# Kernel tuning notes

Hardware: AMD Instinct MI355X
Metric: run time of the kernel (lower is better)

Reference implementation:

```python
import jax, jax.numpy as jnp
import numpy as np

B, S, D, H = 4, 2048, 512, 16
HD = D // H          # head_dim = 32
ROPE_DIM = HD        # rope_pct = 1.0
NEG = -1e30


def apply_rope(x):
    # x: [B, H, S, HD]; rotate first ROPE_DIM dims, half-split (NeoX) convention
    half = ROPE_DIM // 2
    pos = jnp.arange(S, dtype=jnp.float32)
    inv_freq = 1.0 / (10000.0 ** (jnp.arange(0, ROPE_DIM, 2, dtype=jnp.float32) / ROPE_DIM))
    ang = pos[:, None] * inv_freq[None, :]          # [S, half]
    cos, sin = jnp.cos(ang), jnp.sin(ang)           # broadcast over B,H
    x1 = x[..., :half]
    x2 = x[..., half:ROPE_DIM]
    r1 = x1 * cos - x2 * sin
    r2 = x2 * cos + x1 * sin
    rest = x[..., ROPE_DIM:]
    return jnp.concatenate([r1, r2, rest], axis=-1)


def setup_inputs() -> dict:
    key = jax.random.key(0)
    ks = jax.random.split(key, 7)
    x = jax.random.normal(ks[0], (B, S, D), dtype=jnp.float32)
    # causal mask: True = block (j > i)
    attn_mask = jnp.triu(jnp.ones((S, S), dtype=bool), k=1)
    # padding mask: True = PAD; random lengths in [S//2, S]
    lengths = jax.random.randint(ks[1], (B,), S // 2, S + 1)
    key_padding_mask = jnp.arange(S)[None, :] >= lengths[:, None]
    scale = D ** -0.5
    Wq = jax.random.normal(ks[2], (D, D), dtype=jnp.float32) * scale
    Wk = jax.random.normal(ks[3], (D, D), dtype=jnp.float32) * scale
    Wv = jax.random.normal(ks[4], (D, D), dtype=jnp.float32) * scale
    Wo = jax.random.normal(ks[5], (D, D), dtype=jnp.float32) * scale
    return {"x": x, "attn_mask": attn_mask, "key_padding_mask": key_padding_mask,
            "Wq": Wq, "Wk": Wk, "Wv": Wv, "Wo": Wo}


def reference(x, attn_mask, key_padding_mask, Wq, Wk, Wv, Wo):
    scale = HD ** -0.5
    # nn.Linear: y = x @ W.T
    q = (x @ Wq.T).reshape(B, S, H, HD).transpose(0, 2, 1, 3)  # [B,H,S,HD]
    k = (x @ Wk.T).reshape(B, S, H, HD).transpose(0, 2, 1, 3)
    v = (x @ Wv.T).reshape(B, S, H, HD).transpose(0, 2, 1, 3)
    q = apply_rope(q)
    k = apply_rope(k)
    scores = jnp.einsum('bhid,bhjd->bhij', q, k) * scale       # [B,H,S,S]
    scores = jnp.where(key_padding_mask[:, None, None, :], NEG, scores)
    scores = jnp.where(attn_mask[None, None, :, :], NEG, scores)
    probs = jax.nn.softmax(scores.astype(jnp.float32), axis=-1)
    probs = jnp.nan_to_num(probs, nan=0.0)
    ctx = jnp.einsum('bhij,bhjd->bhid', probs, v)              # [B,H,S,HD]
    ctx = ctx.transpose(0, 2, 1, 3).reshape(B, S, D)
    ctx = jnp.where(key_padding_mask[:, :, None], 0.0, ctx)
    return ctx @ Wo.T
```

## Files before the change

### kernel.cpp

```cpp
#include <hip/hip_runtime.h>
#include <hip/hip_bf16.h>

#define B_ 4
#define S_ 2048
#define D_ 512
#define H_ 16
#define HD_ 32

typedef __bf16 bf16;
typedef __bf16 bf16x4 __attribute__((ext_vector_type(4)));
typedef __bf16 bf16x8 __attribute__((ext_vector_type(8)));
typedef float f32x4 __attribute__((ext_vector_type(4)));

__device__ __forceinline__ f32x4 mfma16(bf16x8 a, bf16x8 b, f32x4 c) {
  return __builtin_amdgcn_mfma_f32_16x16x32_bf16(a, b, c, 0, 0, 0);
}

__device__ __forceinline__ void gload16(const bf16* g, bf16* l) {
  __builtin_amdgcn_global_load_lds(
      (const __attribute__((address_space(1))) void*)g,
      (__attribute__((address_space(3))) void*)l, 16, 0, 0);
}

__device__ __forceinline__ bf16x8 cvt8(const float* __restrict__ p) {
  const f32x4* v = (const f32x4*)p;
  f32x4 a = v[0], b = v[1];
  bf16x8 r;
  r[0] = (bf16)a[0]; r[1] = (bf16)a[1]; r[2] = (bf16)a[2]; r[3] = (bf16)a[3];
  r[4] = (bf16)b[0]; r[5] = (bf16)b[1]; r[6] = (bf16)b[2]; r[7] = (bf16)b[3];
  return r;
}

__global__ __launch_bounds__(256) void prep_kernel(
    const float* __restrict__ x, const float* __restrict__ wq,
    const float* __restrict__ wk, const float* __restrict__ wv,
    const float* __restrict__ wo, const unsigned char* __restrict__ am,
    const unsigned char* __restrict__ kpm, bf16* __restrict__ xb,
    bf16* __restrict__ dq, bf16* __restrict__ dk, bf16* __restrict__ dv,
    bf16* __restrict__ dwo, int* __restrict__ lengths_out,
    float* __restrict__ costab, float* __restrict__ sintab) {
  int bid = blockIdx.x;
  if (bid < 2048) {
    size_t i = (size_t)bid * 256 + threadIdx.x;
    *(bf16x8*)(xb + i * 8) = cvt8(x + i * 8);
  } else if (bid < 2560) {
    int wb = bid - 2048;
    int mat = wb >> 7;
    size_t i = (size_t)(wb & 127) * 256 + threadIdx.x;
    const float* s = (mat == 0) ? wq : (mat == 1) ? wk : (mat == 2) ? wv : wo;
    bf16* d = (mat == 0) ? dq : (mat == 1) ? dk : (mat == 2) ? dv : dwo;
    *(bf16x8*)(d + i * 8) = cvt8(s + i * 8);
  } else if (bid == 2560) {
    int b = threadIdx.x >> 6, lane = threadIdx.x & 63;
    int esize;
    if (am[1] == 1) esize = 1;
    else if (am[2] == 0x80 && am[3] == 0x3F) esize = 2;
    else if (am[3] == 0x3C) esize = 2;
    else if (am[4] == 1) esize = 4;
    else if (am[6] == 0x80 && am[7] == 0x3F) esize = 4;
    else if (am[8] == 1) esize = 8;
    else esize = 1;
    int cnt = 0;
    for (int i = lane; i < S_; i += 64) {
      size_t off = ((size_t)b * S_ + i) * (size_t)esize;
      unsigned char nz = 0;
      for (int e = 0; e < esize; ++e) nz |= kpm[off + e];
      cnt += (nz == 0) ? 1 : 0;
    }
    for (int off = 1; off < 64; off <<= 1) cnt += __shfl_xor(cnt, off);
    if (lane == 0) lengths_out[b] = cnt;
  } else {
    int ti = (bid - 2561) * 256 + threadIdx.x;
    int s = ti >> 4, cc = ti & 15;
    float invf = powf(10000.0f, -(float)cc * (1.0f / 16.0f));
    float ang = (float)s * invf;
    costab[ti] = cosf(ang);
    sintab[ti] = sinf(ang);
  }
}

#define LDT 136
__global__ __launch_bounds__(256) void qkv_rope_kernel(
    const bf16* __restrict__ x, const bf16* __restrict__ Wq,
    const bf16* __restrict__ Wk, const bf16* __restrict__ Wv,
    const float* __restrict__ costab, const float* __restrict__ sintab,
    bf16* __restrict__ q_ws, bf16* __restrict__ k_ws, bf16* __restrict__ vt_ws) {
  __shared__ __align__(16) bf16 smem[17408];
#define AS(b) (smem + (b) * 4096)
#define BS(b) (smem + 8192 + (b) * 4096)
#define CT smem

  int bid = blockIdx.x;
  int brow = bid / 12, bc = bid % 12;
  int mat = bc >> 2;
  const bf16* W = (mat == 0) ? Wq : (mat == 1) ? Wk : Wv;
  int row0 = brow * 128;
  int col0 = (bc & 3) * 128;

  int tid = threadIdx.x;
  int w = tid >> 6, l = tid & 63;
  int wr = w >> 1, wc = w & 1;
  int g = l >> 4, c = l & 15;
  int lrow = l >> 2;
  int lcol = (l & 3) * 8;

  f32x4 acc[4][4];
  f32x4 zero = {0.f, 0.f, 0.f, 0.f};
#pragma unroll
  for (int m = 0; m < 4; ++m)
#pragma unroll
    for (int n = 0; n < 4; ++n) acc[m][n] = zero;

#pragma unroll
  for (int j = 0; j < 2; ++j) {
    int chunk = w * 2 + j;
    int grow = chunk * 16 + lrow;
    gload16(x + (size_t)(row0 + grow) * 512 + lcol, AS(0) + chunk * 512);
    gload16(W + (size_t)(col0 + grow) * 512 + lcol, BS(0) + chunk * 512);
  }
  __syncthreads();
  int cur = 0;

#pragma unroll 1
  for (int k0 = 0; k0 < 512; k0 += 32) {
    bool more = (k0 < 480);
    if (more) {
#pragma unroll
      for (int j = 0; j < 2; ++j) {
        int chunk = w * 2 + j;
        int grow = chunk * 16 + lrow;
        gload16(x + (size_t)(row0 + grow) * 512 + k0 + 32 + lcol,
                AS(cur ^ 1) + chunk * 512);
        gload16(W + (size_t)(col0 + grow) * 512 + k0 + 32 + lcol,
                BS(cur ^ 1) + chunk * 512);
      }
    }
    bf16x8 af[4], bfr[4];
#pragma unroll
    for (int m = 0; m < 4; ++m)
      af[m] = *(const bf16x8*)(AS(cur) + (wr * 64 + m * 16 + c) * 32 + g * 8);
#pragma unroll
    for (int n = 0; n < 4; ++n)
      bfr[n] = *(const bf16x8*)(BS(cur) + (wc * 64 + n * 16 + c) * 32 + g * 8);
#pragma unroll
    for (int m = 0; m < 4; ++m)
#pragma unroll
      for (int n = 0; n < 4; ++n) acc[m][n] = mfma16(af[m], bfr[n], acc[m][n]);
    if (more) {
      __syncthreads();
      cur ^= 1;
    }
  }

  if (mat < 2) {
    bf16* dst = (mat == 0) ? q_ws : k_ws;
    const float esc =
        (mat == 0) ? (0.17677669529663687f * 1.4426950408889634f) : 1.0f;
#pragma unroll
    for (int m = 0; m < 4; ++m) {
      int rbase = row0 + wr * 64 + m * 16 + g * 4;
#pragma unroll
      for (int r = 0; r < 4; ++r) {
        int grow = rbase + r;
        int bb = grow >> 11, s = grow & (S_ - 1);
        float cs = costab[s * 16 + c];
        float sn = sintab[s * 16 + c];
#pragma unroll
        for (int np = 0; np < 2; ++np) {
          int n = np * 2;
          int obase = col0 + wc * 64 + n * 16;
          int h = obase >> 5;
          float a0 = acc[m][n][r], a1 = acc[m][n + 1][r];
          size_t base = (((size_t)bb * H_ + h) * S_ + s) * HD_;
          dst[base + c] = (bf16)((a0 * cs - a1 * sn) * esc);
          dst[base + c + 16] = (bf16)((a1 * cs + a0 * sn) * esc);
        }
      }
    }
  } else {
    __syncthreads();
#pragma unroll
    for (int m = 0; m < 4; ++m) {
#pragma unroll
      for (int n = 0; n < 4; ++n) {
        int o = wc * 64 + n * 16 + c;
        int sb = wr * 64 + m * 16 + g * 4;
        bf16x4 q4;
        q4[0] = (bf16)acc[m][n][0]; q4[1] = (bf16)acc[m][n][1];
        q4[2] = (bf16)acc[m][n][2]; q4[3] = (bf16)acc[m][n][3];
        *(bf16x4*)(&CT[o * LDT + sb]) = q4;
      }
    }
    __syncthreads();
    int o_l = tid >> 1, sh = (tid & 1) * 64;
    int o = col0 + o_l;
    int h = o >> 5, hd = o & 31;
    int bb2 = row0 >> 11, sr = row0 & (S_ - 1);
    size_t dst = (((size_t)bb2 * H_ + h) * HD_ + hd) * S_ + sr + sh;
#pragma unroll
    for (int j = 0; j < 8; ++j)
      *(bf16x8*)(vt_ws + dst + j * 8) =
          *(const bf16x8*)(&CT[o_l * LDT + sh + j * 8]);
  }
#undef AS
#undef BS
#undef CT
}

__global__ __launch_bounds__(256) void attn_kernel(
    const bf16* __restrict__ q_ws, const bf16* __restrict__ k_ws,
    const bf16* __restrict__ vt_ws, const int* __restrict__ lengths,
    bf16* __restrict__ ctx_ws) {
  __shared__ __align__(16) bf16 Ks[2][2048];
  __shared__ __align__(16) bf16 Vts[2][2048];
  __shared__ __align__(16) bf16 Ps[4][1024];

  int p = blockIdx.x;
  int bh = blockIdx.y;
  int bb = bh >> 4, h = bh & 15;
  int tid = threadIdx.x, w = tid >> 6, l = tid & 63, g = l >> 4, c = l & 15;
  const size_t bh_base = ((size_t)bb * H_ + h) * (size_t)S_ * HD_;
  int len = lengths[bb];
  int rowrel = w * 16 + c;

  int srowK = w * 16 + (l & 15), skgK = l >> 4;
  int srowV = w * 8 + (l & 7), ssgV = l >> 3;
  int slotK8 = (skgK * 16 + (srowK & 15) + ((srowK >> 4) << 6)) * 8;
  int slotV8 =
      ((ssgV & 3) * 16 + (srowV & 15) + (((ssgV >> 2) + ((srowV >> 4) << 1)) << 6)) * 8;

  bf16 one = (bf16)1.0f;
  bf16x8 onesf;
#pragma unroll
  for (int i = 0; i < 8; ++i) onesf[i] = one;

#pragma unroll 1
  for (int phase = 0; phase < 2; ++phase) {
    int qt = phase ? (31 - p) : p;
    int q0 = qt * 64 + w * 16;

    bf16x8 qf = *(const bf16x8*)(q_ws + bh_base + (size_t)(q0 + c) * HD_ + g * 8);

    f32x4 zero = {0.f, 0.f, 0.f, 0.f};
    f32x4 ctxa[2];
    ctxa[0] = zero; ctxa[1] = zero;
    f32x4 lsum = zero;

    const bf16* kptr = k_ws + bh_base + (size_t)srowK * HD_ + skgK * 8;
    const bf16* vptr = vt_ws + bh_base + (size_t)srowV * S_ + ssgV * 8;

    bf16x8 regK = *(const bf16x8*)kptr;
    bf16x8 regV = *(const bf16x8*)vptr;
    kptr += 64 * HD_;
    vptr += 64;
    __syncthreads();
    *(bf16x8*)(&Ks[0][slotK8]) = regK;
    *(bf16x8*)(&Vts[0][slotV8]) = regV;
    __syncthreads();
    int cur = 0;

#pragma unroll 1
    for (int kt = 0; kt <= qt; ++kt) {
      bool hasNext = (kt < qt);
      if (hasNext) {
        regK = *(const bf16x8*)kptr;
        regV = *(const bf16x8*)vptr;
        kptr += 64 * HD_;
        vptr += 64;
      }
      const bf16* KsC = Ks[cur];
      const bf16* VtsC = Vts[cur];

      f32x4 sacc[4];
#pragma unroll
      for (int n = 0; n < 4; ++n) {
        bf16x8 kf = *(const bf16x8*)(&KsC[(l + (n << 6)) * 8]);
        sacc[n] = mfma16(kf, qf, zero);
      }

      float sv[4][4];
      if (kt != qt) {
#pragma unroll
        for (int n = 0; n < 4; ++n)
#pragma unroll
          for (int r = 0; r < 4; ++r)
            sv[n][r] = __builtin_amdgcn_exp2f(sacc[n][r]);
      } else {
#pragma unroll
        for (int n = 0; n < 4; ++n) {
          int jr = n * 16 + g * 4;
#pragma unroll
          for (int r = 0; r < 4; ++r) {
            float e = __builtin_amdgcn_exp2f(sacc[n][r]);
            sv[n][r] = (jr + r > rowrel) ? 0.f : e;
          }
        }
      }

#pragma unroll
      for (int n = 0; n < 4; ++n) {
        bf16x4 pk;
        pk[0] = (bf16)sv[n][0]; pk[1] = (bf16)sv[n][1];
        pk[2] = (bf16)sv[n][2]; pk[3] = (bf16)sv[n][3];
        int chunk = 2 * n + (g >> 1);
        int off = ((chunk >> 2) << 9) + ((chunk & 3) * 16 + c) * 8 + ((g & 1) << 2);
        *(bf16x4*)(&Ps[w][off]) = pk;
      }

      bf16x8 pf0 = *(const bf16x8*)(&Ps[w][l * 8]);
      bf16x8 pf1 = *(const bf16x8*)(&Ps[w][512 + l * 8]);

      lsum = mfma16(pf0, onesf, lsum);
      lsum = mfma16(pf1, onesf, lsum);

#pragma unroll
      for (int n2 = 0; n2 < 2; ++n2) {
        bf16x8 v0 = *(const bf16x8*)(&VtsC[(l + ((2 * n2) << 6)) * 8]);
        bf16x8 v1 = *(const bf16x8*)(&VtsC[(l + ((1 + 2 * n2) << 6)) * 8]);
        ctxa[n2] = mfma16(pf0, v0, ctxa[n2]);
        ctxa[n2] = mfma16(pf1, v1, ctxa[n2]);
      }

      if (hasNext) {
        *(bf16x8*)(&Ks[cur ^ 1][slotK8]) = regK;
        *(bf16x8*)(&Vts[cur ^ 1][slotV8]) = regV;
        __syncthreads();
        cur ^= 1;
      }
    }

#pragma unroll
    for (int n = 0; n < 2; ++n)
#pragma unroll
      for (int r = 0; r < 4; ++r) {
        int qr = q0 + g * 4 + r;
        float val = ctxa[n][r] / lsum[r];
        if (qr >= len) val = 0.f;
        ctx_ws[(((size_t)bb * S_ + qr) * H_ + h) * HD_ + n * 16 + c] = (bf16)val;
      }
  }
}

__global__ __launch_bounds__(256) void out_proj_kernel(
    const bf16* __restrict__ ctx, const bf16* __restrict__ Wo,
    float* __restrict__ out) {
  __shared__ __align__(16) bf16 As[2][4096];
  __shared__ __align__(16) bf16 Bs[2][4096];

  int bid = blockIdx.x;
  int brow = bid >> 2, bc = bid & 3;
  int row0 = brow * 128, col0 = bc * 128;
  int tid = threadIdx.x;
  int w = tid >> 6, l = tid & 63;
  int wr = w >> 1, wc = w & 1;
  int g = l >> 4, c = l & 15;
  int lrow = l >> 2;
  int lcol = (l & 3) * 8;

  f32x4 acc[4][4];
  f32x4 zero = {0.f, 0.f, 0.f, 0.f};
#pragma unroll
  for (int m = 0; m < 4; ++m)
#pragma unroll
    for (int n = 0; n < 4; ++n) acc[m][n] = zero;

#pragma unroll
  for (int j = 0; j < 2; ++j) {
    int chunk = w * 2 + j;
    int grow = chunk * 16 + lrow;
    gload16(ctx + (size_t)(row0 + grow) * 512 + lcol, As[0] + chunk * 512);
    gload16(Wo + (size_t)(col0 + grow) * 512 + lcol, Bs[0] + chunk * 512);
  }
  __syncthreads();
  int cur = 0;

#pragma unroll 1
  for (int k0 = 0; k0 < 512; k0 += 32) {
    bool more = (k0 < 480);
    if (more) {
#pragma unroll
      for (int j = 0; j < 2; ++j) {
        int chunk = w * 2 + j;
        int grow = chunk * 16 + lrow;
        gload16(ctx + (size_t)(row0 + grow) * 512 + k0 + 32 + lcol,
                As[cur ^ 1] + chunk * 512);
        gload16(Wo + (size_t)(col0 + grow) * 512 + k0 + 32 + lcol,
                Bs[cur ^ 1] + chunk * 512);
      }
    }
    bf16x8 af[4], bfr[4];
#pragma unroll
    for (int m = 0; m < 4; ++m)
      af[m] = *(const bf16x8*)(As[cur] + (wr * 64 + m * 16 + c) * 32 + g * 8);
#pragma unroll
    for (int n = 0; n < 4; ++n)
      bfr[n] = *(const bf16x8*)(Bs[cur] + (wc * 64 + n * 16 + c) * 32 + g * 8);
#pragma unroll
    for (int m = 0; m < 4; ++m)
#pragma unroll
      for (int n = 0; n < 4; ++n) acc[m][n] = mfma16(af[m], bfr[n], acc[m][n]);
    if (more) {
      __syncthreads();
      cur ^= 1;
    }
  }

#pragma unroll
  for (int m = 0; m < 4; ++m) {
    int rbase = row0 + wr * 64 + m * 16 + g * 4;
#pragma unroll
    for (int n = 0; n < 4; ++n) {
      int o = col0 + wc * 64 + n * 16 + c;
#pragma unroll
      for (int r = 0; r < 4; ++r)
        out[(size_t)(rbase + r) * 512 + o] = acc[m][n][r];
    }
  }
}

extern "C" void kernel_launch(void* const* d_in, const int* in_sizes, int n_in,
                              void* d_out, int out_size, void* d_ws,
                              size_t ws_size, hipStream_t stream) {
  const float* x = (const float*)d_in[0];
  const unsigned char* am = (const unsigned char*)d_in[1];
  const unsigned char* kpm = (const unsigned char*)d_in[2];
  const float* Wq = (const float*)d_in[3];
  const float* Wk = (const float*)d_in[4];
  const float* Wv = (const float*)d_in[5];
  const float* Wo = (const float*)d_in[6];
  float* out = (float*)d_out;

  char* ws = (char*)d_ws;
  int* lengths = (int*)ws;
  const size_t QKV_ELEMS = (size_t)B_ * H_ * S_ * HD_;
  const size_t W_ELEMS = (size_t)D_ * D_;
  bf16* xb = (bf16*)(ws + 256);
  bf16* q_ws = xb + QKV_ELEMS;
  bf16* k_ws = q_ws + QKV_ELEMS;
  bf16* vt_ws = k_ws + QKV_ELEMS;
  bf16* wqb = vt_ws + QKV_ELEMS;
  bf16* wkb = wqb + W_ELEMS;
  bf16* wvb = wkb + W_ELEMS;
  bf16* wob = wvb + W_ELEMS;
  float* costab = (float*)(wob + W_ELEMS);
  float* sintab = costab + (size_t)S_ * 16;
  bf16* ctx_ws = xb;

  hipLaunchKernelGGL(prep_kernel, dim3(2689), dim3(256), 0, stream, x, Wq, Wk,
                     Wv, Wo, am, kpm, xb, wqb, wkb, wvb, wob, lengths, costab,
                     sintab);
  hipLaunchKernelGGL(qkv_rope_kernel, dim3(768), dim3(256), 0, stream, xb, wqb,
                     wkb, wvb, costab, sintab, q_ws, k_ws, vt_ws);
  hipLaunchKernelGGL(attn_kernel, dim3(16, 64), dim3(256), 0, stream, q_ws, k_ws,
                     vt_ws, lengths, ctx_ws);
  hipLaunchKernelGGL(out_proj_kernel, dim3(256), dim3(256), 0, stream, ctx_ws,
                     wob, out);
}
```

Before: 122.0 us.

## Stage two KV tiles per barrier in attention; halve out-proj row tile

```diff
diff --git a/kernel.cpp b/kernel.cpp
--- a/kernel.cpp
+++ b/kernel.cpp
@@ -211,8 +211,8 @@
     const bf16* __restrict__ q_ws, const bf16* __restrict__ k_ws,
     const bf16* __restrict__ vt_ws, const int* __restrict__ lengths,
     bf16* __restrict__ ctx_ws) {
-  __shared__ __align__(16) bf16 Ks[2][2048];
-  __shared__ __align__(16) bf16 Vts[2][2048];
+  __shared__ __align__(16) bf16 Ks[2][4096];
+  __shared__ __align__(16) bf16 Vts[2][4096];
   __shared__ __align__(16) bf16 Ps[4][1024];
 
   int p = blockIdx.x;
@@ -238,6 +238,7 @@
   for (int phase = 0; phase < 2; ++phase) {
     int qt = phase ? (31 - p) : p;
     int q0 = qt * 64 + w * 16;
+    int T = qt + 1;
 
     bf16x8 qf = *(const bf16x8*)(q_ws + bh_base + (size_t)(q0 + c) * HD_ + g * 8);
 
@@ -246,31 +247,27 @@
     ctxa[0] = zero; ctxa[1] = zero;
     f32x4 lsum = zero;
 
-    const bf16* kptr = k_ws + bh_base + (size_t)srowK * HD_ + skgK * 8;
-    const bf16* vptr = vt_ws + bh_base + (size_t)srowV * S_ + ssgV * 8;
-
-    bf16x8 regK = *(const bf16x8*)kptr;
-    bf16x8 regV = *(const bf16x8*)vptr;
-    kptr += 64 * HD_;
-    vptr += 64;
+    const bf16* kbase = k_ws + bh_base + (size_t)srowK * HD_ + skgK * 8;
+    const bf16* vbase = vt_ws + bh_base + (size_t)srowV * S_ + ssgV * 8;
+
+    bf16x8 rK0 = *(const bf16x8*)kbase;
+    bf16x8 rV0 = *(const bf16x8*)vbase;
+    bf16x8 rK1 = rK0, rV1 = rV0;
+    if (T > 1) {
+      rK1 = *(const bf16x8*)(kbase + 64 * HD_);
+      rV1 = *(const bf16x8*)(vbase + 64);
+    }
     __syncthreads();
-    *(bf16x8*)(&Ks[0][slotK8]) = regK;
-    *(bf16x8*)(&Vts[0][slotV8]) = regV;
+    *(bf16x8*)(&Ks[0][slotK8]) = rK0;
+    *(bf16x8*)(&Vts[0][slotV8]) = rV0;
+    *(bf16x8*)(&Ks[0][2048 + slotK8]) = rK1;
+    *(bf16x8*)(&Vts[0][2048 + slotV8]) = rV1;
     __syncthreads();
     int cur = 0;
 
-#pragma unroll 1
-    for (int kt = 0; kt <= qt; ++kt) {
-      bool hasNext = (kt < qt);
-      if (hasNext) {
-        regK = *(const bf16x8*)kptr;
-        regV = *(const bf16x8*)vptr;
-        kptr += 64 * HD_;
-        vptr += 64;
-      }
-      const bf16* KsC = Ks[cur];
-      const bf16* VtsC = Vts[cur];
-
+    auto body = [&](int t, int off) {
+      const bf16* KsC = &Ks[cur][off];
+      const bf16* VtsC = &Vts[cur][off];
       f32x4 sacc[4];
 #pragma unroll
       for (int n = 0; n < 4; ++n) {
@@ -279,7 +276,7 @@
       }
 
       float sv[4][4];
-      if (kt != qt) {
+      if (t != qt) {
 #pragma unroll
         for (int n = 0; n < 4; ++n)
 #pragma unroll
@@ -303,8 +300,8 @@
         pk[0] = (bf16)sv[n][0]; pk[1] = (bf16)sv[n][1];
         pk[2] = (bf16)sv[n][2]; pk[3] = (bf16)sv[n][3];
         int chunk = 2 * n + (g >> 1);
-        int off = ((chunk >> 2) << 9) + ((chunk & 3) * 16 + c) * 8 + ((g & 1) << 2);
-        *(bf16x4*)(&Ps[w][off]) = pk;
+        int poff = ((chunk >> 2) << 9) + ((chunk & 3) * 16 + c) * 8 + ((g & 1) << 2);
+        *(bf16x4*)(&Ps[w][poff]) = pk;
       }
 
       bf16x8 pf0 = *(const bf16x8*)(&Ps[w][l * 8]);
@@ -320,13 +317,29 @@
         ctxa[n2] = mfma16(pf0, v0, ctxa[n2]);
         ctxa[n2] = mfma16(pf1, v1, ctxa[n2]);
       }
-
-      if (hasNext) {
-        *(bf16x8*)(&Ks[cur ^ 1][slotK8]) = regK;
-        *(bf16x8*)(&Vts[cur ^ 1][slotV8]) = regV;
-        __syncthreads();
-        cur ^= 1;
-      }
+    };
+
+#pragma unroll 1
+    for (int r = 0;; ++r) {
+      int t0 = 2 * r, t1 = 2 * r + 1;
+      bool more = (t0 + 2 < T);
+      if (more) {
+        const bf16* kp = kbase + (size_t)(t0 + 2) * 64 * HD_;
+        const bf16* vp = vbase + (t0 + 2) * 64;
+        rK0 = *(const bf16x8*)kp;
+        rV0 = *(const bf16x8*)vp;
+        rK1 = *(const bf16x8*)(kp + 64 * HD_);
+        rV1 = *(const bf16x8*)(vp + 64);
+      }
+      body(t0, 0);
+      if (t1 < T) body(t1, 2048);
+      if (!more) break;
+      *(bf16x8*)(&Ks[cur ^ 1][slotK8]) = rK0;
+      *(bf16x8*)(&Vts[cur ^ 1][slotV8]) = rV0;
+      *(bf16x8*)(&Ks[cur ^ 1][2048 + slotK8]) = rK1;
+      *(bf16x8*)(&Vts[cur ^ 1][2048 + slotV8]) = rV1;
+      __syncthreads();
+      cur ^= 1;
     }
 
 #pragma unroll
@@ -344,12 +357,12 @@
 __global__ __launch_bounds__(256) void out_proj_kernel(
     const bf16* __restrict__ ctx, const bf16* __restrict__ Wo,
     float* __restrict__ out) {
-  __shared__ __align__(16) bf16 As[2][4096];
+  __shared__ __align__(16) bf16 As[2][2048];
   __shared__ __align__(16) bf16 Bs[2][4096];
 
   int bid = blockIdx.x;
   int brow = bid >> 2, bc = bid & 3;
-  int row0 = brow * 128, col0 = bc * 128;
+  int row0 = brow * 64, col0 = bc * 128;
   int tid = threadIdx.x;
   int w = tid >> 6, l = tid & 63;
   int wr = w >> 1, wc = w & 1;
@@ -357,19 +370,22 @@
   int lrow = l >> 2;
   int lcol = (l & 3) * 8;
 
-  f32x4 acc[4][4];
+  f32x4 acc[2][4];
   f32x4 zero = {0.f, 0.f, 0.f, 0.f};
 #pragma unroll
-  for (int m = 0; m < 4; ++m)
+  for (int m = 0; m < 2; ++m)
 #pragma unroll
     for (int n = 0; n < 4; ++n) acc[m][n] = zero;
 
 #pragma unroll
-  for (int j = 0; j < 2; ++j) {
-    int chunk = w * 2 + j;
-    int grow = chunk * 16 + lrow;
-    gload16(ctx + (size_t)(row0 + grow) * 512 + lcol, As[0] + chunk * 512);
-    gload16(Wo + (size_t)(col0 + grow) * 512 + lcol, Bs[0] + chunk * 512);
+  for (int j = 0; j < 3; ++j) {
+    int chunk = w * 3 + j;
+    if (chunk < 4)
+      gload16(ctx + (size_t)(row0 + chunk * 16 + lrow) * 512 + lcol,
+              As[0] + chunk * 512);
+    else
+      gload16(Wo + (size_t)(col0 + (chunk - 4) * 16 + lrow) * 512 + lcol,
+              Bs[0] + (chunk - 4) * 512);
   }
   __syncthreads();
   int cur = 0;
@@ -379,24 +395,26 @@
     bool more = (k0 < 480);
     if (more) {
 #pragma unroll
-      for (int j = 0; j < 2; ++j) {
-        int chunk = w * 2 + j;
-        int grow = chunk * 16 + lrow;
-        gload16(ctx + (size_t)(row0 + grow) * 512 + k0 + 32 + lcol,
-                As[cur ^ 1] + chunk * 512);
-        gload16(Wo + (size_t)(col0 + grow) * 512 + k0 + 32 + lcol,
-                Bs[cur ^ 1] + chunk * 512);
-      }
-    }
-    bf16x8 af[4], bfr[4];
-#pragma unroll
-    for (int m = 0; m < 4; ++m)
-      af[m] = *(const bf16x8*)(As[cur] + (wr * 64 + m * 16 + c) * 32 + g * 8);
+      for (int j = 0; j < 3; ++j) {
+        int chunk = w * 3 + j;
+        if (chunk < 4)
+          gload16(ctx + (size_t)(row0 + chunk * 16 + lrow) * 512 + k0 + 32 + lcol,
+                  As[cur ^ 1] + chunk * 512);
+        else
+          gload16(Wo + (size_t)(col0 + (chunk - 4) * 16 + lrow) * 512 + k0 + 32 +
+                      lcol,
+                  Bs[cur ^ 1] + (chunk - 4) * 512);
+      }
+    }
+    bf16x8 af[2], bfr[4];
+#pragma unroll
+    for (int m = 0; m < 2; ++m)
+      af[m] = *(const bf16x8*)(As[cur] + (wr * 32 + m * 16 + c) * 32 + g * 8);
 #pragma unroll
     for (int n = 0; n < 4; ++n)
       bfr[n] = *(const bf16x8*)(Bs[cur] + (wc * 64 + n * 16 + c) * 32 + g * 8);
 #pragma unroll
-    for (int m = 0; m < 4; ++m)
+    for (int m = 0; m < 2; ++m)
 #pragma unroll
       for (int n = 0; n < 4; ++n) acc[m][n] = mfma16(af[m], bfr[n], acc[m][n]);
     if (more) {
@@ -406,8 +424,8 @@
   }
 
 #pragma unroll
-  for (int m = 0; m < 4; ++m) {
-    int rbase = row0 + wr * 64 + m * 16 + g * 4;
+  for (int m = 0; m < 2; ++m) {
+    int rbase = row0 + wr * 32 + m * 16 + g * 4;
 #pragma unroll
     for (int n = 0; n < 4; ++n) {
       int o = col0 + wc * 64 + n * 16 + c;
@@ -453,6 +471,6 @@
                      wkb, wvb, costab, sintab, q_ws, k_ws, vt_ws);
   hipLaunchKernelGGL(attn_kernel, dim3(16, 64), dim3(256), 0, stream, q_ws, k_ws,
                      vt_ws, lengths, ctx_ws);
-  hipLaunchKernelGGL(out_proj_kernel, dim3(256), dim3(256), 0, stream, ctx_ws,
+  hipLaunchKernelGGL(out_proj_kernel, dim3(512), dim3(256), 0, stream, ctx_ws,
                      wob, out);
 }
```

Result: faster. 118.8 us (-2.6%).
